# Kernel optimization log

Measured on AMD Instinct MI355X. Metric: run time of the kernel, lower is better.

## Reference

```python
import jax, jax.numpy as jnp
import numpy as np

B, FX1, K, H, W = 4, 64, 80, 64, 64
G, GH = 5, 5  # num_groups, head_gn_groups
GATE_SCALE = 0.1
EPS = 1e-5


def conv2d(x, w, pad=0):
    # x: [B,C,H,W], w: [O,I,kh,kw]
    return jax.lax.conv_general_dilated(
        x, w, window_strides=(1, 1), padding=[(pad, pad), (pad, pad)],
        dimension_numbers=('NCHW', 'OIHW', 'NCHW'))


def group_norm(x, gamma, beta, groups):
    b, c, h, w = x.shape
    xg = x.reshape(b, groups, c // groups, h, w)
    m = xg.mean(axis=(2, 3, 4), keepdims=True)
    v = xg.var(axis=(2, 3, 4), keepdims=True)
    xn = ((xg - m) * jax.lax.rsqrt(v + EPS)).reshape(b, c, h, w)
    return xn * gamma[None, :, None, None] + beta[None, :, None, None]


def layer_norm(x, gamma, beta):
    m = x.mean(axis=-1, keepdims=True)
    v = x.var(axis=-1, keepdims=True)
    return (x - m) * jax.lax.rsqrt(v + EPS) * gamma + beta


def setup_inputs() -> dict:
    key = jax.random.key(0)
    ks = jax.random.split(key, 20)
    s = 0.05
    d = {
        'x1': jax.random.normal(ks[0], (B, FX1, H, W), jnp.float32),
        'x2': jax.random.normal(ks[1], (B, K, H, W), jnp.float32),
        # proj_x1: conv3x3 + GN + SiLU
        'w_p1': s * jax.random.normal(ks[2], (K, FX1, 3, 3), jnp.float32),
        'gn1_g': jnp.ones((K,), jnp.float32), 'gn1_b': jnp.zeros((K,), jnp.float32),
        # proj_x2_id: conv1x1 + GN
        'w_id': s * jax.random.normal(ks[3], (K, K, 1, 1), jnp.float32),
        'gnid_g': jnp.ones((K,), jnp.float32), 'gnid_b': jnp.zeros((K,), jnp.float32),
        # q,k,v linear weights [out,in]
        'wq': s * jax.random.normal(ks[4], (K, K), jnp.float32),
        'wk': s * jax.random.normal(ks[5], (K, K), jnp.float32),
        'wv': s * jax.random.normal(ks[6], (K, K), jnp.float32),
        # gate: conv3x3 -> GN -> SiLU -> conv1x1(+bias)
        'wg1': s * jax.random.normal(ks[7], (K // 2, K, 3, 3), jnp.float32),
        'gng_g': jnp.ones((K // 2,), jnp.float32), 'gng_b': jnp.zeros((K // 2,), jnp.float32),
        'wg2': s * jax.random.normal(ks[8], (K, K // 2, 1, 1), jnp.float32),
        'bg2': jnp.zeros((K,), jnp.float32),
        # layernorms
        'lnx1_g': jnp.ones((K,), jnp.float32), 'lnx1_b': jnp.zeros((K,), jnp.float32),
        'lnx2_g': jnp.ones((K,), jnp.float32), 'lnx2_b': jnp.zeros((K,), jnp.float32),
        'lno_g': jnp.ones((K,), jnp.float32), 'lno_b': jnp.zeros((K,), jnp.float32),
        # head (conv3x3 mode): conv3x3 -> GN -> SiLU -> conv1x1(+bias=0)
        'wh1': s * jax.random.normal(ks[9], (K, K, 3, 3), jnp.float32),
        'gnh_g': jnp.ones((K,), jnp.float32), 'gnh_b': jnp.zeros((K,), jnp.float32),
        'wh2': s * jax.random.normal(ks[10], (1, K, 1, 1), jnp.float32),
        'bh2': jnp.zeros((1,), jnp.float32),
    }
    return d


def reference(x1, x2, w_p1, gn1_g, gn1_b, w_id, gnid_g, gnid_b, wq, wk, wv,
              wg1, gng_g, gng_b, wg2, bg2, lnx1_g, lnx1_b, lnx2_g, lnx2_b,
              lno_g, lno_b, wh1, gnh_g, gnh_b, wh2, bh2):
    b, _, h, w = x1.shape
    hw = h * w
    # proj_x1: conv3x3 + GN + SiLU  -> [B,K,H,W]
    x1p = jax.nn.silu(group_norm(conv2d(x1, w_p1, pad=1), gn1_g, gn1_b, G))
    # proj_x2_id: conv1x1 + GN
    x2_id = group_norm(conv2d(x2, w_id), gnid_g, gnid_b, G)
    # to sequences [B, HW, K]
    x1s = layer_norm(x1p.reshape(b, K, hw).transpose(0, 2, 1), lnx1_g, lnx1_b)
    x2s = layer_norm(x2.reshape(b, K, hw).transpose(0, 2, 1), lnx2_g, lnx2_b)
    q = jnp.einsum('bnk,ok->bno', x1s, wq)
    kk = jnp.einsum('bnk,ok->bno', x2s, wk)
    v = jnp.einsum('bnk,ok->bno', x2s, wv)
    # gate branch
    g = jax.nn.silu(group_norm(conv2d(x2, wg1, pad=1), gng_g, gng_b, G))
    g = conv2d(g, wg2) + bg2[None, :, None, None]
    g = jax.nn.sigmoid(g).reshape(b, K, hw).transpose(0, 2, 1)
    v = v * (1.0 + GATE_SCALE * g)
    # dense attention over HW tokens
    attn = jnp.einsum('bnk,bmk->bnm', q, kk) / jnp.sqrt(jnp.float32(K)).astype(q.dtype)
    attn = jax.nn.softmax(attn, axis=-1)
    y = jnp.einsum('bnm,bmk->bnk', attn, v)
    x2_id_seq = x2_id.reshape(b, K, hw).transpose(0, 2, 1)
    y = layer_norm(y + x2_id_seq, lno_g, lno_b)
    # head: conv3x3 -> GN -> SiLU -> conv1x1
    y_map = y.transpose(0, 2, 1).reshape(b, K, h, w)
    hmid = jax.nn.silu(group_norm(conv2d(y_map, wh1, pad=1), gnh_g, gnh_b, GH))
    logits = (conv2d(hmid, wh2) + bh2[None, :, None, None]).reshape(b, hw)
    pred = jax.nn.sigmoid(logits)
    xmin = jnp.min(x2, axis=1).reshape(b, hw)
    return pred, xmin
```

## Files before the change

kernel.cpp:

```cpp
#include <hip/hip_runtime.h>
#include <hip/hip_bf16.h>
#include <math.h>

#define BSZ 4
#define CK 80
#define CX1 64
#define CGT 40
#define HH 64
#define WWI 64
#define HWSZ 4096
#define NGRP 5
#define EPSV 1e-5f
#define SPLIT 8
#define KPB (HWSZ / SPLIT)
#define NCH (KPB / 32)
#define PADHW 4356

typedef short bf16x8 __attribute__((ext_vector_type(8)));
typedef float f32x16 __attribute__((ext_vector_type(16)));
#define MFMA32(a, b, c) __builtin_amdgcn_mfma_f32_32x32x16_bf16(a, b, c, 0, 0, 0)

__device__ __forceinline__ float sigmoidf_(float x) { return 1.f / (1.f + __expf(-x)); }
__device__ __forceinline__ float siluf_(float x) { return x * sigmoidf_(x); }

__device__ __forceinline__ ushort f2bf(float x) {
  union { float f; uint u; } c;
  c.f = x;
  uint u = c.u;
  return (ushort)((u + 0x7FFFu + ((u >> 16) & 1u)) >> 16);
}
__device__ __forceinline__ uint pack2bf(float lo, float hi) {
  return (uint)f2bf(lo) | ((uint)f2bf(hi) << 16);
}
__device__ __forceinline__ float bf2f(ushort u) {
  union { uint u; float f; } c;
  c.u = ((uint)u) << 16;
  return c.f;
}
__device__ __forceinline__ bf16x8 as_bf8(uint4 v) {
  union { uint4 u; bf16x8 b; } c;
  c.u = v;
  return c.b;
}
__device__ __forceinline__ bf16x8 ldb8(const ushort* p) { return *(const bf16x8*)p; }

__device__ __forceinline__ void repack_one(const float* w, ushort* wt, int idx, int COUT,
                                           int CIN, int TAPS, int COP) {
  int tap = idx / (COP * CIN);
  int rem = idx - tap * COP * CIN;
  int co = rem / CIN, ci = rem - co * CIN;
  float v = (co < COUT) ? w[((size_t)co * CIN + ci) * TAPS + tap] : 0.f;
  wt[idx] = f2bf(v);
}
__device__ __forceinline__ void zero_one(ushort* buf, int u, int cin) {
  int nu = cin >> 1;
  int pid = u / nu, uoff = u - pid * nu;
  int b = pid / 260, pos = pid - b * 260;
  int h, w;
  if (pos < 66) { h = 0; w = pos; }
  else if (pos < 132) { h = 65; w = pos - 66; }
  else if (pos < 196) { h = pos - 131; w = 0; }
  else { h = pos - 195; w = 65; }
  ((uint*)(buf + (((size_t)b * PADHW) + h * 66 + w) * cin))[uoff] = 0;
}
__device__ __forceinline__ void repack_lin(const float* w, ushort* wt, int idx, int COUT,
                                           int CIN, float scale) {
  int co = idx / CIN, ci = idx - co * CIN;
  float v = (co < COUT) ? w[(size_t)co * CIN + ci] * scale : 0.f;
  wt[idx] = f2bf(v);
}
__global__ __launch_bounds__(256) void setup_k(const float* __restrict__ w_p1,
                                               const float* __restrict__ w_id,
                                               const float* __restrict__ wg1,
                                               const float* __restrict__ wh1,
                                               const float* __restrict__ wq,
                                               const float* __restrict__ wk,
                                               const float* __restrict__ wv,
                                               const float* __restrict__ wg2,
                                               ushort* wp1t, ushort* widt, ushort* wg1t,
                                               ushort* wh1t, ushort* wqt, ushort* wkt,
                                               ushort* wvt, ushort* wg2t, ushort* x1_tm,
                                               ushort* x2_tm, ushort* ym_tm) {
  int idx = blockIdx.x * 256 + threadIdx.x;
  if (idx < 55296) repack_one(w_p1, wp1t, idx, 80, 64, 9, 96);
  else if (idx < 62976) repack_one(w_id, widt, idx - 55296, 80, 80, 1, 96);
  else if (idx < 109056) repack_one(wg1, wg1t, idx - 62976, 40, 80, 9, 64);
  else if (idx < 178176) repack_one(wh1, wh1t, idx - 109056, 80, 80, 9, 96);
  else if (idx < 211456) zero_one(x1_tm, idx - 178176, CX1);
  else if (idx < 253056) zero_one(x2_tm, idx - 211456, CK);
  else if (idx < 294656) zero_one(ym_tm, idx - 253056, CK);
  else if (idx < 302336)
    repack_lin(wq, wqt, idx - 294656, 80, 80, 0.111803398874989485f);
  else if (idx < 310016) repack_lin(wk, wkt, idx - 302336, 80, 80, 1.f);
  else if (idx < 317696) repack_lin(wv, wvt, idx - 310016, 80, 80, 1.f);
  else if (idx < 322304) {
    int i2 = idx - 317696;
    int co = i2 / 48, ci = i2 - co * 48;
    float v = (co < 80 && ci < 40) ? wg2[(size_t)co * 40 + ci] : 0.f;
    wg2t[i2] = f2bf(v);
  }
}

template <int CIN>
__device__ __forceinline__ void stage_body(const float* __restrict__ in,
                                           ushort* __restrict__ xtm,
                                           float (*tile)[81]) {
  int h = blockIdx.x, b = blockIdx.y;
  int w = threadIdx.x & 63, cio = threadIdx.x >> 6;
  for (int ci = cio; ci < CIN; ci += 4)
    tile[w][ci] = in[((size_t)(b * CIN + ci)) * HWSZ + h * 64 + w];
  __syncthreads();
  const int PAIRS = CIN / 2;
  for (int idx = threadIdx.x; idx < 64 * PAIRS; idx += 256) {
    int wi = idx / PAIRS, cp = idx - wi * PAIRS;
    uint pk = pack2bf(tile[wi][2 * cp], tile[wi][2 * cp + 1]);
    *(uint*)(&xtm[(((size_t)b * PADHW) + (h + 1) * 66 + (wi + 1)) * CIN + 2 * cp]) = pk;
  }
}
__global__ __launch_bounds__(256) void stage2_k(const float* __restrict__ x1,
                                                const float* __restrict__ x2,
                                                ushort* __restrict__ x1_tm,
                                                ushort* __restrict__ x2_tm) {
  __shared__ float tile[64][81];
  if (blockIdx.z == 0) stage_body<CX1>(x1, x1_tm, tile);
  else stage_body<CK>(x2, x2_tm, tile);
}

template <int CIN, int COP, int TAPS, int COUT>
__device__ __forceinline__ void conv_body(const ushort* __restrict__ xtm,
                                          const ushort* __restrict__ wt,
                                          float* __restrict__ out, int tile, int nt,
                                          float* lds) {
  int lane = threadIdx.x;
  int half = lane >> 5, lq = lane & 31;
  int b = tile >> 7;
  int tstart = (tile & 127) * 32;
  int h = tstart >> 6, w0 = tstart & 63;
  int p0 = (h + 1) * 66 + (w0 + lq + 1);
  const ushort* xb = xtm + ((size_t)b * PADHW) * CIN;
  const ushort* wbase = wt + ((size_t)(nt * 32 + lq)) * CIN + half * 8;
  f32x16 acc;
#pragma unroll
  for (int i = 0; i < 16; ++i) acc[i] = 0.f;
#pragma unroll 3
  for (int tap = 0; tap < TAPS; ++tap) {
    int dtap = (TAPS == 1) ? 0 : ((tap / 3) - 1) * 66 + (tap % 3) - 1;
    const ushort* ap = xb + (size_t)(p0 + dtap) * CIN + half * 8;
    const ushort* wp = wbase + (size_t)tap * COP * CIN;
#pragma unroll
    for (int kc = 0; kc < CIN / 16; ++kc) {
      acc = MFMA32(ldb8(ap + kc * 16), ldb8(wp + kc * 16), acc);
    }
  }
#pragma unroll
  for (int r = 0; r < 16; ++r) {
    int m = (r & 3) + 8 * (r >> 2) + 4 * half;
    lds[m * 33 + lq] = acc[r];
  }
  __syncthreads();
#pragma unroll
  for (int i = 0; i < 16; ++i) {
    int idx = i * 64 + lane;
    int c2 = idx >> 5, m2 = idx & 31;
    int co = nt * 32 + c2;
    if (co < COUT) out[((size_t)b * COUT + co) * HWSZ + tstart + m2] = lds[m2 * 33 + c2];
  }
}

__global__ __launch_bounds__(64) void convA_k(const ushort* __restrict__ x1_tm,
                                              const ushort* __restrict__ x2_tm,
                                              const ushort* __restrict__ wp1t,
                                              const ushort* __restrict__ widt,
                                              const ushort* __restrict__ wg1t,
                                              float* __restrict__ c1,
                                              float* __restrict__ xid,
                                              float* __restrict__ cg1) {
  __shared__ float lds[32 * 33];
  int zy = blockIdx.y;
  if (zy < 3) conv_body<CX1, 96, 9, CK>(x1_tm, wp1t, c1, blockIdx.x, zy, lds);
  else if (zy < 6) conv_body<CK, 96, 1, CK>(x2_tm, widt, xid, blockIdx.x, zy - 3, lds);
  else conv_body<CK, 64, 9, CGT>(x2_tm, wg1t, cg1, blockIdx.x, zy - 6, lds);
}

__global__ __launch_bounds__(64) void convH_k(const ushort* __restrict__ ym_tm,
                                              const ushort* __restrict__ wh1t,
                                              float* __restrict__ ch1) {
  __shared__ float lds[32 * 33];
  conv_body<CK, 96, 9, CK>(ym_tm, wh1t, ch1, blockIdx.x, blockIdx.y, lds);
}

__device__ __forceinline__ void gn_part_body(const float* __restrict__ x,
                                             float* __restrict__ pstat, int C, int cpg) {
  int bg = blockIdx.x;
  int sl = blockIdx.y;
  int g = bg % NGRP, b = bg / NGRP;
  int npb = cpg * HWSZ / 16;
  const float4* p =
      (const float4*)(x + ((size_t)b * C + (size_t)g * cpg) * HWSZ + (size_t)sl * npb);
  int n4 = npb / 4;
  float s = 0.f, s2 = 0.f;
  for (int i = threadIdx.x; i < n4; i += 256) {
    float4 v = p[i];
    s += v.x + v.y + v.z + v.w;
    s2 += v.x * v.x + v.y * v.y + v.z * v.z + v.w * v.w;
  }
#pragma unroll
  for (int off = 32; off; off >>= 1) {
    s += __shfl_down(s, off);
    s2 += __shfl_down(s2, off);
  }
  __shared__ float sh[4][2];
  int wave = threadIdx.x >> 6;
  if ((threadIdx.x & 63) == 0) {
    sh[wave][0] = s;
    sh[wave][1] = s2;
  }
  __syncthreads();
  if (threadIdx.x == 0) {
    pstat[bg * 32 + sl * 2] = sh[0][0] + sh[1][0] + sh[2][0] + sh[3][0];
    pstat[bg * 32 + sl * 2 + 1] = sh[0][1] + sh[1][1] + sh[2][1] + sh[3][1];
  }
}
__global__ __launch_bounds__(256) void gnA_k(const float* __restrict__ c1,
                                             const float* __restrict__ xid,
                                             const float* __restrict__ cg1,
                                             float* __restrict__ pst1,
                                             float* __restrict__ pstid,
                                             float* __restrict__ pstg) {
  int z = blockIdx.z;
  if (z == 0) gn_part_body(c1, pst1, CK, 16);
  else if (z == 1) gn_part_body(xid, pstid, CK, 16);
  else gn_part_body(cg1, pstg, CGT, 8);
}
__global__ __launch_bounds__(256) void gnH_k(const float* __restrict__ ch1,
                                             float* __restrict__ psth) {
  gn_part_body(ch1, psth, CK, 16);
}

__device__ __forceinline__ void gn_fin_lds(const float* __restrict__ ps, int b, float invn,
                                           int tid, float* gsm, float* gsr) {
  if (tid < NGRP) {
    const float* p = ps + ((size_t)(b * NGRP + tid)) * 32;
    float s = 0.f, s2 = 0.f;
#pragma unroll
    for (int sl = 0; sl < 16; ++sl) {
      s += p[sl * 2];
      s2 += p[sl * 2 + 1];
    }
    float m = s * invn;
    gsm[tid] = m;
    gsr[tid] = rsqrtf(fmaxf(s2 * invn - m * m, 0.f) + EPSV);
  }
}

__global__ __launch_bounds__(512) void norm_k(const float* __restrict__ c1,
                                              const float* __restrict__ x2,
                                              const float* __restrict__ cg1,
                                              const float* __restrict__ pst1,
                                              const float* __restrict__ pstg,
                                              const float* __restrict__ gn1_g,
                                              const float* __restrict__ gn1_b,
                                              const float* __restrict__ gng_g,
                                              const float* __restrict__ gng_b,
                                              const float* __restrict__ lnx1_g,
                                              const float* __restrict__ lnx1_b,
                                              const float* __restrict__ lnx2_g,
                                              const float* __restrict__ lnx2_b,
                                              ushort* __restrict__ x1n,
                                              ushort* __restrict__ x2n,
                                              ushort* __restrict__ gsi) {
  __shared__ float xs[64][85];
  __shared__ float mrs[64][2];
  __shared__ float gsm[NGRP], gsr[NGRP];
  int tid = threadIdx.x, tl = tid & 63, g = tid >> 6;
  int b = blockIdx.y, n0 = blockIdx.x * 64;
  int z = blockIdx.z;

  if (z == 2) {
    gn_fin_lds(pstg, b, 1.f / (8 * HWSZ), tid, gsm, gsr);
    __syncthreads();
    ushort* gp = gsi + ((size_t)(b * HWSZ) + n0 + tl) * 48;
#pragma unroll
    for (int j = 0; j < 6; j += 2) {
      int c = g * 6 + j;
      float v0 = 0.f, v1 = 0.f;
      if (c < CGT) {
        int gr = c >> 3;
        v0 = siluf_((cg1[((size_t)(b * CGT + c)) * HWSZ + n0 + tl] - gsm[gr]) * gsr[gr] *
                        gng_g[c] +
                    gng_b[c]);
      }
      if (c + 1 < CGT) {
        int gr = (c + 1) >> 3;
        v1 = siluf_((cg1[((size_t)(b * CGT + c + 1)) * HWSZ + n0 + tl] - gsm[gr]) *
                        gsr[gr] * gng_g[c + 1] +
                    gng_b[c + 1]);
      }
      *(uint*)(gp + c) = pack2bf(v0, v1);
    }
    return;
  }

  if (z == 0) {
    gn_fin_lds(pst1, b, 1.f / (16 * HWSZ), tid, gsm, gsr);
    __syncthreads();
#pragma unroll
    for (int j = 0; j < 10; ++j) {
      int c = g * 10 + j;
      int gr = c >> 4;
      float v = (c1[((size_t)(b * CK + c)) * HWSZ + n0 + tl] - gsm[gr]) * gsr[gr] *
                    gn1_g[c] +
                gn1_b[c];
      xs[tl][c] = siluf_(v);
    }
  } else {
#pragma unroll
    for (int j = 0; j < 10; ++j) {
      int c = g * 10 + j;
      xs[tl][c] = x2[((size_t)(b * CK + c)) * HWSZ + n0 + tl];
    }
  }
  __syncthreads();
  if (tid < 64) {
    float s = 0.f, s2 = 0.f;
#pragma unroll
    for (int c = 0; c < CK; ++c) {
      float v = xs[tid][c];
      s += v;
      s2 += v * v;
    }
    float mean = s * (1.f / CK);
    float var = s2 * (1.f / CK) - mean * mean;
    mrs[tid][0] = mean;
    mrs[tid][1] = rsqrtf(var + EPSV);
  }
  __syncthreads();
  float mean = mrs[tl][0], rstd = mrs[tl][1];
  const float* lg = (z == 0) ? lnx1_g : lnx2_g;
  const float* lb = (z == 0) ? lnx1_b : lnx2_b;
  ushort* op = ((z == 0) ? x1n : x2n) + ((size_t)(b * HWSZ) + n0 + tl) * CK;
#pragma unroll
  for (int j = 0; j < 10; j += 2) {
    int c = g * 10 + j;
    float v0 = (xs[tl][c] - mean) * rstd * lg[c] + lb[c];
    float v1 = (xs[tl][c + 1] - mean) * rstd * lg[c + 1] + lb[c + 1];
    *(uint*)(op + c) = pack2bf(v0, v1);
  }
}

__global__ __launch_bounds__(64) void qkvg_k(const ushort* __restrict__ x1n,
                                             const ushort* __restrict__ x2n,
                                             const ushort* __restrict__ gsi,
                                             const ushort* __restrict__ wqt,
                                             const ushort* __restrict__ wkt,
                                             const ushort* __restrict__ wvt,
                                             const ushort* __restrict__ wg2t,
                                             const float* __restrict__ bg2,
                                             ushort* __restrict__ qb,
                                             ushort* __restrict__ kb,
                                             ushort* __restrict__ vt) {
  __shared__ float lds[32 * 33];
  int lane = threadIdx.x;
  int half = lane >> 5, lq = lane & 31;
  int tile = blockIdx.x, zy = blockIdx.y;
  int seg = zy / 3, nt = zy - seg * 3;
  int b = tile >> 7;
  int tstart = (tile & 127) * 32;

  if (seg < 2) {
    const ushort* xn = (seg == 0) ? x1n : x2n;
    const ushort* wt = (seg == 0) ? wqt : wkt;
    ushort* outb = (seg == 0) ? qb : kb;
    const ushort* ap = xn + ((size_t)(b * HWSZ) + tstart + lq) * CK + half * 8;
    const ushort* wp = wt + (size_t)(nt * 32 + lq) * CK + half * 8;
    f32x16 acc;
#pragma unroll
    for (int i = 0; i < 16; ++i) acc[i] = 0.f;
#pragma unroll
    for (int kc = 0; kc < 5; ++kc)
      acc = MFMA32(ldb8(ap + kc * 16), ldb8(wp + kc * 16), acc);
#pragma unroll
    for (int r = 0; r < 16; ++r) {
      int m = (r & 3) + 8 * (r >> 2) + 4 * half;
      lds[m * 33 + lq] = acc[r];
    }
    __syncthreads();
#pragma unroll
    for (int i = 0; i < 8; ++i) {
      int idx = i * 64 + lane;
      int tok = idx >> 4, pr = idx & 15;
      int co = nt * 32 + pr * 2;
      if (co < CK) {
        uint pk = pack2bf(lds[tok * 33 + pr * 2], lds[tok * 33 + pr * 2 + 1]);
        *(uint*)(&outb[((size_t)(b * HWSZ) + tstart + tok) * CK + co]) = pk;
      }
    }
  } else {
    const ushort* ap = x2n + ((size_t)(b * HWSZ) + tstart + lq) * CK + half * 8;
    const ushort* gp = gsi + ((size_t)(b * HWSZ) + tstart + lq) * 48 + half * 8;
    const ushort* wvp = wvt + (size_t)(nt * 32 + lq) * CK + half * 8;
    const ushort* wgp = wg2t + (size_t)(nt * 32 + lq) * 48 + half * 8;
    f32x16 vacc, gacc;
#pragma unroll
    for (int i = 0; i < 16; ++i) { vacc[i] = 0.f; gacc[i] = 0.f; }
#pragma unroll
    for (int kc = 0; kc < 5; ++kc)
      vacc = MFMA32(ldb8(ap + kc * 16), ldb8(wvp + kc * 16), vacc);
#pragma unroll
    for (int kc = 0; kc < 3; ++kc)
      gacc = MFMA32(ldb8(gp + kc * 16), ldb8(wgp + kc * 16), gacc);
    int co = nt * 32 + lq;
    float bias = (co < CK) ? bg2[co] : 0.f;
#pragma unroll
    for (int r = 0; r < 16; ++r) {
      int m = (r & 3) + 8 * (r >> 2) + 4 * half;
      float gv = 1.f + 0.1f * sigmoidf_(gacc[r] + bias);
      lds[m * 33 + lq] = vacc[r] * gv;
    }
    __syncthreads();
#pragma unroll
    for (int i = 0; i < 16; ++i) {
      int idx = i * 64 + lane;
      int c2 = idx >> 5, m2 = idx & 31;
      int co2 = nt * 32 + c2;
      vt[((size_t)(b * 96 + co2)) * HWSZ + tstart + m2] = f2bf(lds[m2 * 33 + c2]);
    }
  }
}

__global__ __launch_bounds__(512) void attn2_k(const ushort* __restrict__ qb,
                                               const ushort* __restrict__ kb,
                                               const ushort* __restrict__ vt,
                                               ushort* __restrict__ part_o,
                                               float* __restrict__ part_l) {
  __shared__ ushort kl[2][2816];
  __shared__ ushort vl[2][3456];
  int tid = threadIdx.x, wid = tid >> 6, lane = tid & 63;
  int half = lane >> 5, lq = lane & 31;
  int qblk = blockIdx.x, b = blockIdx.y, ks = blockIdx.z;
  int k00 = ks * KPB;

  const ushort* qp =
      qb + ((size_t)b * HWSZ + qblk * 256 + wid * 32 + lq) * CK + half * 8;
  bf16x8 qf0 = *(const bf16x8*)(qp);
  bf16x8 qf1 = *(const bf16x8*)(qp + 16);
  bf16x8 qf2 = *(const bf16x8*)(qp + 32);
  bf16x8 qf3 = *(const bf16x8*)(qp + 48);
  bf16x8 qf4 = *(const bf16x8*)(qp + 64);

  f32x16 oa[3];
#pragma unroll
  for (int dt = 0; dt < 3; ++dt)
#pragma unroll
    for (int i = 0; i < 16; ++i) oa[dt][i] = 0.f;
  float lsum = 0.f;

  const ushort* kgb = kb + (size_t)b * HWSZ * CK;
  const ushort* vgb = vt + (size_t)b * 96 * HWSZ;

  uint4 kreg;
  uint2 vreg0, vreg1;
  int ktok = tid / 10, kgc = tid - ktok * 10;
  int vr0 = tid >> 3, vgc0 = tid & 7;
  int vr1 = (512 + tid) >> 3, vgc1 = tid & 7;

  auto load_stage = [&](int ch) {
    int k0 = k00 + ch * 32;
    const ushort* kg = kgb + (size_t)k0 * CK;
    if (tid < 320) kreg = *(const uint4*)(kg + (size_t)ktok * CK + kgc * 8);
    vreg0 = *(const uint2*)(vgb + (size_t)vr0 * HWSZ + k0 + vgc0 * 4);
    if (tid < 256) vreg1 = *(const uint2*)(vgb + (size_t)vr1 * HWSZ + k0 + vgc1 * 4);
  };
  auto write_stage = [&](int buf) {
    if (tid < 320) *(uint4*)(&kl[buf][ktok * 88 + kgc * 8]) = kreg;
    *(uint2*)(&vl[buf][vr0 * 36 + vgc0 * 4]) = vreg0;
    if (tid < 256) *(uint2*)(&vl[buf][vr1 * 36 + vgc1 * 4]) = vreg1;
  };

  load_stage(0);
  write_stage(0);
  __syncthreads();

  for (int c = 0; c < NCH; ++c) {
    int cur = c & 1;
    if (c + 1 < NCH) load_stage(c + 1);

    const ushort* klp = &kl[cur][lq * 88 + half * 8];
    f32x16 s;
#pragma unroll
    for (int i = 0; i < 16; ++i) s[i] = 0.f;
    s = MFMA32(*(const bf16x8*)(klp), qf0, s);
    s = MFMA32(*(const bf16x8*)(klp + 16), qf1, s);
    s = MFMA32(*(const bf16x8*)(klp + 32), qf2, s);
    s = MFMA32(*(const bf16x8*)(klp + 48), qf3, s);
    s = MFMA32(*(const bf16x8*)(klp + 64), qf4, s);

    uint w[8];
#pragma unroll
    for (int i = 0; i < 8; ++i) {
      float e0 = __expf(s[2 * i]);
      float e1 = __expf(s[2 * i + 1]);
      lsum += e0 + e1;
      __hip_bfloat162 t = __float22bfloat162_rn(make_float2(e0, e1));
      union { __hip_bfloat162 h; uint u; } cv;
      cv.h = t;
      w[i] = cv.u;
    }
    uint4 pw0 = make_uint4(w[0], w[1], w[2], w[3]);
    uint4 pw1 = make_uint4(w[4], w[5], w[6], w[7]);

#pragma unroll
    for (int dt = 0; dt < 3; ++dt) {
      const ushort* vp = &vl[cur][(dt * 32 + lq) * 36 + half * 4];
      uint2 a0 = *(const uint2*)(vp);
      uint2 b0 = *(const uint2*)(vp + 8);
      uint2 a1 = *(const uint2*)(vp + 16);
      uint2 b1 = *(const uint2*)(vp + 24);
      oa[dt] = MFMA32(as_bf8(make_uint4(a0.x, a0.y, b0.x, b0.y)), as_bf8(pw0), oa[dt]);
      oa[dt] = MFMA32(as_bf8(make_uint4(a1.x, a1.y, b1.x, b1.y)), as_bf8(pw1), oa[dt]);
    }
    if (c + 1 < NCH) write_stage(cur ^ 1);
    __syncthreads();
  }

  float ltot = lsum + __shfl_xor(lsum, 32);
  size_t tileidx = (size_t)((b * 128 + qblk * 8 + wid) * SPLIT + ks);
  ushort* po = part_o + tileidx * 2560;
#pragma unroll
  for (int dt = 0; dt < 3; ++dt)
#pragma unroll
    for (int r = 0; r < 16; ++r) {
      int d = dt * 32 + (r & 3) + 8 * (r >> 2) + 4 * half;
      if (d < CK) po[d * 32 + lq] = f2bf(oa[dt][r]);
    }
  if (lane < 32) part_l[tileidx * 32 + lq] = ltot;
}

__global__ __launch_bounds__(512) void post2_k(const ushort* __restrict__ part_o,
                                               const float* __restrict__ part_l,
                                               const float* __restrict__ xid,
                                               const float* __restrict__ pstid,
                                               const float* __restrict__ gg,
                                               const float* __restrict__ gb,
                                               const float* __restrict__ lg,
                                               const float* __restrict__ lb,
                                               ushort* __restrict__ ym_tm) {
  __shared__ float xs[64][85];
  __shared__ float mrs[64][2];
  __shared__ float gsm[NGRP], gsr[NGRP];
  __shared__ float invl[64];
  int tid = threadIdx.x, tl = tid & 63, g = tid >> 6;
  int b = blockIdx.y, n0 = blockIdx.x * 64;
  gn_fin_lds(pstid, b, 1.f / (16 * HWSZ), tid, gsm, gsr);
  if (tid < 64) {
    int token = n0 + tid;
    int qt = token >> 5, lqq = token & 31;
    size_t tb = (size_t)(b * 128 + qt) * SPLIT;
    float s = 0.f;
#pragma unroll
    for (int sp = 0; sp < SPLIT; ++sp) s += part_l[(tb + sp) * 32 + lqq];
    invl[tid] = 1.f / s;
  }
  __syncthreads();
  {
    int token = n0 + tl;
    int qt = token >> 5, lqq = token & 31;
    size_t tb = (size_t)(b * 128 + qt) * SPLIT;
    float il = invl[tl];
#pragma unroll
    for (int j = 0; j < 10; ++j) {
      int c = g * 10 + j;
      int gr = c >> 4;
      float y = 0.f;
#pragma unroll
      for (int sp = 0; sp < SPLIT; ++sp)
        y += bf2f(part_o[(tb + sp) * 2560 + c * 32 + lqq]);
      y *= il;
      xs[tl][c] = y + ((xid[((size_t)(b * CK + c)) * HWSZ + n0 + tl] - gsm[gr]) * gsr[gr] *
                           gg[c] +
                       gb[c]);
    }
  }
  __syncthreads();
  if (tid < 64) {
    float s = 0.f, s2 = 0.f;
#pragma unroll
    for (int c = 0; c < CK; ++c) {
      float v = xs[tid][c];
      s += v;
      s2 += v * v;
    }
    float mean = s * (1.f / CK);
    float var = s2 * (1.f / CK) - mean * mean;
    mrs[tid][0] = mean;
    mrs[tid][1] = rsqrtf(var + EPSV);
  }
  __syncthreads();
  float mean = mrs[tl][0], rstd = mrs[tl][1];
#pragma unroll
  for (int j = 0; j < 10; ++j) {
    int c = g * 10 + j;
    xs[tl][c] = (xs[tl][c] - mean) * rstd * lg[c] + lb[c];
  }
  __syncthreads();
  int hh = n0 >> 6;
  ushort* op = ym_tm + (((size_t)b * PADHW) + (hh + 1) * 66 + 1) * CK;
  for (int idx = tid; idx < 640; idx += 512) {
    int w = idx / 10, q4 = idx - w * 10;
    const float* xp = &xs[w][q4 * 8];
    uint4 pk;
    pk.x = pack2bf(xp[0], xp[1]);
    pk.y = pack2bf(xp[2], xp[3]);
    pk.z = pack2bf(xp[4], xp[5]);
    pk.w = pack2bf(xp[6], xp[7]);
    *(uint4*)(op + (size_t)w * CK + q4 * 8) = pk;
  }
}

__global__ __launch_bounds__(512) void final_k(const float* __restrict__ ch1,
                                               const float* __restrict__ psth,
                                               const float* __restrict__ gg,
                                               const float* __restrict__ gb,
                                               const float* __restrict__ wh2,
                                               const float* __restrict__ bh2,
                                               const float* __restrict__ x2,
                                               float* __restrict__ out) {
  __shared__ float pd[64][9];
  __shared__ float pm[64][9];
  __shared__ float gsm[NGRP], gsr[NGRP];
  int tid = threadIdx.x, tl = tid & 63, g = tid >> 6;
  int b = blockIdx.y, n0 = blockIdx.x * 64;
  gn_fin_lds(psth, b, 1.f / (16 * HWSZ), tid, gsm, gsr);
  __syncthreads();
  float acc = 0.f, mn = 3.4e38f;
#pragma unroll
  for (int j = 0; j < 10; ++j) {
    int c = g * 10 + j;
    int gr = c >> 4;
    float v = (ch1[((size_t)(b * CK + c)) * HWSZ + n0 + tl] - gsm[gr]) * gsr[gr] * gg[c] +
              gb[c];
    acc += siluf_(v) * wh2[c];
    mn = fminf(mn, x2[((size_t)(b * CK + c)) * HWSZ + n0 + tl]);
  }
  pd[tl][g] = acc;
  pm[tl][g] = mn;
  __syncthreads();
  if (tid < 64) {
    float a = bh2[0];
    float m = pm[tid][0];
#pragma unroll
    for (int g2 = 0; g2 < 8; ++g2) a += pd[tid][g2];
#pragma unroll
    for (int g2 = 1; g2 < 8; ++g2) m = fminf(m, pm[tid][g2]);
    out[(size_t)b * HWSZ + n0 + tid] = sigmoidf_(a);
    out[(size_t)BSZ * HWSZ + (size_t)b * HWSZ + n0 + tid] = m;
  }
}

extern "C" void kernel_launch(void* const* d_in, const int* in_sizes, int n_in,
                              void* d_out, int out_size, void* d_ws, size_t ws_size,
                              hipStream_t stream) {
  const float* x1 = (const float*)d_in[0];
  const float* x2 = (const float*)d_in[1];
  const float* w_p1 = (const float*)d_in[2];
  const float* gn1_g = (const float*)d_in[3];
  const float* gn1_b = (const float*)d_in[4];
  const float* w_id = (const float*)d_in[5];
  const float* gnid_g = (const float*)d_in[6];
  const float* gnid_b = (const float*)d_in[7];
  const float* wq = (const float*)d_in[8];
  const float* wk = (const float*)d_in[9];
  const float* wv = (const float*)d_in[10];
  const float* wg1 = (const float*)d_in[11];
  const float* gng_g = (const float*)d_in[12];
  const float* gng_b = (const float*)d_in[13];
  const float* wg2 = (const float*)d_in[14];
  const float* bg2 = (const float*)d_in[15];
  const float* lnx1_g = (const float*)d_in[16];
  const float* lnx1_b = (const float*)d_in[17];
  const float* lnx2_g = (const float*)d_in[18];
  const float* lnx2_b = (const float*)d_in[19];
  const float* lno_g = (const float*)d_in[20];
  const float* lno_b = (const float*)d_in[21];
  const float* wh1 = (const float*)d_in[22];
  const float* gnh_g = (const float*)d_in[23];
  const float* gnh_b = (const float*)d_in[24];
  const float* wh2 = (const float*)d_in[25];
  const float* bh2 = (const float*)d_in[26];
  (void)in_sizes; (void)n_in; (void)out_size; (void)ws_size;

  float* ws = (float*)d_ws;
  float* c1 = ws;
  float* xid = c1 + 1310720;
  float* cg1 = xid + 1310720;
  float* ch1 = cg1 + 655360;
  ushort* part_o = (ushort*)(ch1 + 1310720);
  float* part_l = (float*)(part_o + 10485760);
  float* pst1 = part_l + 131072;
  float* pstid = pst1 + 640;
  float* pstg = pstid + 640;
  float* psth = pstg + 640;
  ushort* qb = (ushort*)(psth + 640);
  ushort* kb = qb + 1310720;
  ushort* vt = kb + 1310720;
  ushort* x1_tm = vt + 1572864;
  ushort* x2_tm = x1_tm + 1115136;
  ushort* ym_tm = x2_tm + 1393920;
  ushort* x1n = ym_tm + 1393920;
  ushort* x2n = x1n + 1310720;
  ushort* gsi = x2n + 1310720;
  ushort* wp1t = gsi + 786432;
  ushort* widt = wp1t + 55296;
  ushort* wg1t = widt + 7680;
  ushort* wh1t = wg1t + 46080;
  ushort* wqt = wh1t + 69120;
  ushort* wkt = wqt + 7680;
  ushort* wvt = wkt + 7680;
  ushort* wg2t = wvt + 7680;

  setup_k<<<dim3(1259), 256, 0, stream>>>(w_p1, w_id, wg1, wh1, wq, wk, wv, wg2, wp1t,
                                          widt, wg1t, wh1t, wqt, wkt, wvt, wg2t, x1_tm,
                                          x2_tm, ym_tm);
  stage2_k<<<dim3(64, BSZ, 2), 256, 0, stream>>>(x1, x2, x1_tm, x2_tm);
  convA_k<<<dim3(512, 8), 64, 0, stream>>>(x1_tm, x2_tm, wp1t, widt, wg1t, c1, xid, cg1);
  gnA_k<<<dim3(BSZ * NGRP, 16, 3), 256, 0, stream>>>(c1, xid, cg1, pst1, pstid, pstg);
  norm_k<<<dim3(64, BSZ, 3), 512, 0, stream>>>(c1, x2, cg1, pst1, pstg, gn1_g, gn1_b,
                                               gng_g, gng_b, lnx1_g, lnx1_b, lnx2_g,
                                               lnx2_b, x1n, x2n, gsi);
  qkvg_k<<<dim3(512, 9), 64, 0, stream>>>(x1n, x2n, gsi, wqt, wkt, wvt, wg2t, bg2, qb, kb,
                                          vt);
  attn2_k<<<dim3(16, BSZ, SPLIT), 512, 0, stream>>>(qb, kb, vt, part_o, part_l);
  post2_k<<<dim3(64, BSZ), 512, 0, stream>>>(part_o, part_l, xid, pstid, gnid_g, gnid_b,
                                             lno_g, lno_b, ym_tm);
  convH_k<<<dim3(512, 3), 64, 0, stream>>>(ym_tm, wh1t, ch1);
  gnH_k<<<dim3(BSZ * NGRP, 16), 256, 0, stream>>>(ch1, psth);
  final_k<<<dim3(64, BSZ), 512, 0, stream>>>(ch1, psth, gnh_g, gnh_b, wh2, bh2, x2,
                                             (float*)d_out);
}
```

Measured before the change: 111.0 us.

## Double attention key chunk to 64 tokens and fold log2e into Q scale

Result: slower. 141.0 us (+27.0%).

```diff
diff --git a/kernel.cpp b/kernel.cpp
--- a/kernel.cpp
+++ b/kernel.cpp
@@ -13,7 +13,8 @@
 #define EPSV 1e-5f
 #define SPLIT 8
 #define KPB (HWSZ / SPLIT)
-#define NCH (KPB / 32)
+#define CHK 64
+#define NCH2 (KPB / CHK)
 #define PADHW 4356
 
 typedef short bf16x8 __attribute__((ext_vector_type(8)));
@@ -90,7 +91,8 @@
   else if (idx < 253056) zero_one(x2_tm, idx - 211456, CK);
   else if (idx < 294656) zero_one(ym_tm, idx - 253056, CK);
   else if (idx < 302336)
-    repack_lin(wq, wqt, idx - 294656, 80, 80, 0.111803398874989485f);
+    repack_lin(wq, wqt, idx - 294656, 80, 80,
+               0.111803398874989485f * 1.4426950408889634f);
   else if (idx < 310016) repack_lin(wk, wkt, idx - 302336, 80, 80, 1.f);
   else if (idx < 317696) repack_lin(wv, wvt, idx - 310016, 80, 80, 1.f);
   else if (idx < 322304) {
@@ -428,13 +430,13 @@
   }
 }
 
-__global__ __launch_bounds__(512) void attn2_k(const ushort* __restrict__ qb,
-                                               const ushort* __restrict__ kb,
-                                               const ushort* __restrict__ vt,
-                                               ushort* __restrict__ part_o,
-                                               float* __restrict__ part_l) {
-  __shared__ ushort kl[2][2816];
-  __shared__ ushort vl[2][3456];
+__global__ __launch_bounds__(512, 4) void attn3_k(const ushort* __restrict__ qb,
+                                                  const ushort* __restrict__ kb,
+                                                  const ushort* __restrict__ vt,
+                                                  ushort* __restrict__ part_o,
+                                                  float* __restrict__ part_l) {
+  __shared__ ushort kl[2][64 * 88];
+  __shared__ ushort vl[2][96 * 68];
   int tid = threadIdx.x, wid = tid >> 6, lane = tid & 63;
   int half = lane >> 5, lq = lane & 31;
   int qblk = blockIdx.x, b = blockIdx.y, ks = blockIdx.z;
@@ -458,68 +460,94 @@
   const ushort* kgb = kb + (size_t)b * HWSZ * CK;
   const ushort* vgb = vt + (size_t)b * 96 * HWSZ;
 
-  uint4 kreg;
-  uint2 vreg0, vreg1;
-  int ktok = tid / 10, kgc = tid - ktok * 10;
-  int vr0 = tid >> 3, vgc0 = tid & 7;
-  int vr1 = (512 + tid) >> 3, vgc1 = tid & 7;
+  int kt0 = tid / 10, kc0 = tid - kt0 * 10;
+  int kt1 = (512 + tid) / 10, kc1 = (512 + tid) - kt1 * 10;
+  int vr0 = tid >> 4, vc = tid & 15;
+
+  uint4 kreg0, kreg1;
+  uint2 vreg0, vreg1, vreg2;
 
   auto load_stage = [&](int ch) {
-    int k0 = k00 + ch * 32;
+    int k0 = k00 + ch * CHK;
     const ushort* kg = kgb + (size_t)k0 * CK;
-    if (tid < 320) kreg = *(const uint4*)(kg + (size_t)ktok * CK + kgc * 8);
-    vreg0 = *(const uint2*)(vgb + (size_t)vr0 * HWSZ + k0 + vgc0 * 4);
-    if (tid < 256) vreg1 = *(const uint2*)(vgb + (size_t)vr1 * HWSZ + k0 + vgc1 * 4);
+    kreg0 = *(const uint4*)(kg + (size_t)kt0 * CK + kc0 * 8);
+    if (tid < 128) kreg1 = *(const uint4*)(kg + (size_t)kt1 * CK + kc1 * 8);
+    vreg0 = *(const uint2*)(vgb + (size_t)vr0 * HWSZ + k0 + vc * 4);
+    vreg1 = *(const uint2*)(vgb + (size_t)(vr0 + 32) * HWSZ + k0 + vc * 4);
+    vreg2 = *(const uint2*)(vgb + (size_t)(vr0 + 64) * HWSZ + k0 + vc * 4);
   };
   auto write_stage = [&](int buf) {
-    if (tid < 320) *(uint4*)(&kl[buf][ktok * 88 + kgc * 8]) = kreg;
-    *(uint2*)(&vl[buf][vr0 * 36 + vgc0 * 4]) = vreg0;
-    if (tid < 256) *(uint2*)(&vl[buf][vr1 * 36 + vgc1 * 4]) = vreg1;
+    *(uint4*)(&kl[buf][kt0 * 88 + kc0 * 8]) = kreg0;
+    if (tid < 128) *(uint4*)(&kl[buf][kt1 * 88 + kc1 * 8]) = kreg1;
+    *(uint2*)(&vl[buf][vr0 * 68 + vc * 4]) = vreg0;
+    *(uint2*)(&vl[buf][(vr0 + 32) * 68 + vc * 4]) = vreg1;
+    *(uint2*)(&vl[buf][(vr0 + 64) * 68 + vc * 4]) = vreg2;
   };
 
   load_stage(0);
   write_stage(0);
   __syncthreads();
 
-  for (int c = 0; c < NCH; ++c) {
+  for (int c = 0; c < NCH2; ++c) {
     int cur = c & 1;
-    if (c + 1 < NCH) load_stage(c + 1);
-
-    const ushort* klp = &kl[cur][lq * 88 + half * 8];
+    if (c + 1 < NCH2) load_stage(c + 1);
+
+    const ushort* klpA = &kl[cur][lq * 88 + half * 8];
     f32x16 s;
 #pragma unroll
     for (int i = 0; i < 16; ++i) s[i] = 0.f;
-    s = MFMA32(*(const bf16x8*)(klp), qf0, s);
-    s = MFMA32(*(const bf16x8*)(klp + 16), qf1, s);
-    s = MFMA32(*(const bf16x8*)(klp + 32), qf2, s);
-    s = MFMA32(*(const bf16x8*)(klp + 48), qf3, s);
-    s = MFMA32(*(const bf16x8*)(klp + 64), qf4, s);
-
-    uint w[8];
+    s = MFMA32(ldb8(klpA), qf0, s);
+    s = MFMA32(ldb8(klpA + 16), qf1, s);
+    s = MFMA32(ldb8(klpA + 32), qf2, s);
+    s = MFMA32(ldb8(klpA + 48), qf3, s);
+    s = MFMA32(ldb8(klpA + 64), qf4, s);
+    uint wA[8];
 #pragma unroll
     for (int i = 0; i < 8; ++i) {
-      float e0 = __expf(s[2 * i]);
-      float e1 = __expf(s[2 * i + 1]);
+      float e0 = exp2f(s[2 * i]);
+      float e1 = exp2f(s[2 * i + 1]);
       lsum += e0 + e1;
-      __hip_bfloat162 t = __float22bfloat162_rn(make_float2(e0, e1));
-      union { __hip_bfloat162 h; uint u; } cv;
-      cv.h = t;
-      w[i] = cv.u;
-    }
-    uint4 pw0 = make_uint4(w[0], w[1], w[2], w[3]);
-    uint4 pw1 = make_uint4(w[4], w[5], w[6], w[7]);
+      wA[i] = pack2bf(e0, e1);
+    }
+    uint4 pwA0 = make_uint4(wA[0], wA[1], wA[2], wA[3]);
+    uint4 pwA1 = make_uint4(wA[4], wA[5], wA[6], wA[7]);
+
+    const ushort* klpB = &kl[cur][(32 + lq) * 88 + half * 8];
+#pragma unroll
+    for (int i = 0; i < 16; ++i) s[i] = 0.f;
+    s = MFMA32(ldb8(klpB), qf0, s);
+    s = MFMA32(ldb8(klpB + 16), qf1, s);
+    s = MFMA32(ldb8(klpB + 32), qf2, s);
+    s = MFMA32(ldb8(klpB + 48), qf3, s);
+    s = MFMA32(ldb8(klpB + 64), qf4, s);
+    uint wB[8];
+#pragma unroll
+    for (int i = 0; i < 8; ++i) {
+      float e0 = exp2f(s[2 * i]);
+      float e1 = exp2f(s[2 * i + 1]);
+      lsum += e0 + e1;
+      wB[i] = pack2bf(e0, e1);
+    }
+    uint4 pwB0 = make_uint4(wB[0], wB[1], wB[2], wB[3]);
+    uint4 pwB1 = make_uint4(wB[4], wB[5], wB[6], wB[7]);
 
 #pragma unroll
     for (int dt = 0; dt < 3; ++dt) {
-      const ushort* vp = &vl[cur][(dt * 32 + lq) * 36 + half * 4];
+      const ushort* vp = &vl[cur][(dt * 32 + lq) * 68 + half * 4];
       uint2 a0 = *(const uint2*)(vp);
       uint2 b0 = *(const uint2*)(vp + 8);
       uint2 a1 = *(const uint2*)(vp + 16);
       uint2 b1 = *(const uint2*)(vp + 24);
-      oa[dt] = MFMA32(as_bf8(make_uint4(a0.x, a0.y, b0.x, b0.y)), as_bf8(pw0), oa[dt]);
-      oa[dt] = MFMA32(as_bf8(make_uint4(a1.x, a1.y, b1.x, b1.y)), as_bf8(pw1), oa[dt]);
-    }
-    if (c + 1 < NCH) write_stage(cur ^ 1);
+      oa[dt] = MFMA32(as_bf8(make_uint4(a0.x, a0.y, b0.x, b0.y)), as_bf8(pwA0), oa[dt]);
+      oa[dt] = MFMA32(as_bf8(make_uint4(a1.x, a1.y, b1.x, b1.y)), as_bf8(pwA1), oa[dt]);
+      uint2 c0 = *(const uint2*)(vp + 32);
+      uint2 d0 = *(const uint2*)(vp + 40);
+      uint2 c1 = *(const uint2*)(vp + 48);
+      uint2 d1 = *(const uint2*)(vp + 56);
+      oa[dt] = MFMA32(as_bf8(make_uint4(c0.x, c0.y, d0.x, d0.y)), as_bf8(pwB0), oa[dt]);
+      oa[dt] = MFMA32(as_bf8(make_uint4(c1.x, c1.y, d1.x, d1.y)), as_bf8(pwB1), oa[dt]);
+    }
+    if (c + 1 < NCH2) write_stage(cur ^ 1);
     __syncthreads();
   }
 
@@ -729,7 +757,7 @@
                                                lnx2_b, x1n, x2n, gsi);
   qkvg_k<<<dim3(512, 9), 64, 0, stream>>>(x1n, x2n, gsi, wqt, wkt, wvt, wg2t, bg2, qb, kb,
                                           vt);
-  attn2_k<<<dim3(16, BSZ, SPLIT), 512, 0, stream>>>(qb, kb, vt, part_o, part_l);
+  attn3_k<<<dim3(16, BSZ, SPLIT), 512, 0, stream>>>(qb, kb, vt, part_o, part_l);
   post2_k<<<dim3(64, BSZ), 512, 0, stream>>>(part_o, part_l, xid, pstid, gnid_g, gnid_b,
                                              lno_g, lno_b, ym_tm);
   convH_k<<<dim3(512, 3), 64, 0, stream>>>(ym_tm, wh1t, ch1);
```
